# Kernel optimization log

Measured on AMD Instinct MI355X. Metric: run time of the kernel, lower is better.

The kernel has to match this reference:

```python
import jax, jax.numpy as jnp
import numpy as np

N, IN_DIM, OUT_DIM, H = 50000, 128, 128, 4
C = OUT_DIM // H  # 32, per-head channels
E = 1_600_000
NEG_SLOPE = 0.2
LN_EPS = 1e-5


def setup_inputs() -> dict:
    key = jax.random.key(0)
    ks = jax.random.split(key, 12)
    x = jax.random.normal(ks[0], (N, IN_DIM), dtype=jnp.float32)
    edge_index = jax.random.randint(ks[1], (2, E), 0, N, dtype=jnp.int64)
    edge_weight = jax.random.uniform(ks[2], (E,), dtype=jnp.float32)
    s = 1.0 / np.sqrt(IN_DIM)
    W = jax.random.normal(ks[3], (IN_DIM, H * C), dtype=jnp.float32) * s
    att_src = jax.random.normal(ks[4], (1, H, C), dtype=jnp.float32) * s
    att_dst = jax.random.normal(ks[5], (1, H, C), dtype=jnp.float32) * s
    W_edge = jax.random.normal(ks[6], (1, H * C), dtype=jnp.float32)
    att_edge = jax.random.normal(ks[7], (1, H, C), dtype=jnp.float32) * s
    bias = jnp.zeros((H * C,), dtype=jnp.float32)
    ln_gamma = jnp.ones((OUT_DIM,), dtype=jnp.float32)
    ln_beta = jnp.zeros((OUT_DIM,), dtype=jnp.float32)
    return {"x": x, "edge_index": edge_index, "edge_weight": edge_weight,
            "W": W, "att_src": att_src, "att_dst": att_dst,
            "W_edge": W_edge, "att_edge": att_edge, "bias": bias,
            "ln_gamma": ln_gamma, "ln_beta": ln_beta}


def _gat_forward(x, edge_index, edge_weight, W, att_src, att_dst, W_edge, att_edge, bias):
    # GATConv(in, C, heads=H, edge_dim=1), concat=True, add_self_loops=True (fill_value='mean')
    xp = (x @ W).reshape(N, H, C)                      # [N,H,C]
    a_src = jnp.sum(xp * att_src, axis=-1)             # [N,H]
    a_dst = jnp.sum(xp * att_dst, axis=-1)             # [N,H]

    # add self-loops; self-loop edge_attr = mean of existing edge_attr
    loop = jnp.arange(N, dtype=edge_index.dtype)
    src = jnp.concatenate([edge_index[0], loop])       # [E+N]
    dst = jnp.concatenate([edge_index[1], loop])
    ew = jnp.concatenate([edge_weight, jnp.full((N,), jnp.mean(edge_weight), edge_weight.dtype)])

    ea = (ew[:, None] @ W_edge).reshape(-1, H, C)      # [E+N,H,C]
    a_edge = jnp.sum(ea * att_edge, axis=-1)           # [E+N,H]

    logits = a_src[src] + a_dst[dst] + a_edge          # [E+N,H]
    logits = jax.nn.leaky_relu(logits, NEG_SLOPE)

    # segment softmax over destination-node neighborhoods
    m = jax.ops.segment_max(logits, dst, num_segments=N)     # [N,H]
    ex = jnp.exp(logits - m[dst])
    denom = jax.ops.segment_sum(ex, dst, num_segments=N)     # [N,H]
    attn = ex / (denom[dst] + 1e-16)                          # [E+N,H]

    msg = attn[:, :, None] * xp[src]                          # [E+N,H,C]
    out = jax.ops.segment_sum(msg, dst, num_segments=N)      # [N,H,C]
    return out.reshape(N, H * C) + bias


def reference(x, edge_index, edge_weight, W, att_src, att_dst, W_edge, att_edge, bias, ln_gamma, ln_beta):
    out = _gat_forward(x, edge_index, edge_weight, W, att_src, att_dst, W_edge, att_edge, bias)
    # LayerNorm
    mu = jnp.mean(out, axis=-1, keepdims=True)
    var = jnp.mean(jnp.square(out - mu), axis=-1, keepdims=True)
    out = (out - mu) / jnp.sqrt(var + LN_EPS) * ln_gamma + ln_beta
    # ELU (dropout is identity in eval)
    return jax.nn.elu(out)
```

## Files before the change

### kernel.cpp

```cpp
#include <hip/hip_runtime.h>
#include <hip/hip_fp16.h>
#include <cstddef>

#define N_NODES 50000
#define E_EDGES 1600000
#define NEG_SLOPE 0.2f
#define LN_EPS 1e-5f
#define LOG2E 1.4426950408889634f
#define PAD 96

#define NBK 782
#define BCAP 2560
#define PCH 4096
#define NCH 391
#define NGB 1563
#define TPB 256

#define OFF_SCAL    0u
#define OFF_BCUR    256u
#define OFF_EWPART  4096u
#define OFF_COUNTS  8192u
#define OFF_ASRC    208256u
#define OFF_ADST    1008256u
#define OFF_XPH     1808256u
#define OFF_PAIRS   14608256u
#define OFF_STAGE   33808256u

#define XROW_B   272
#define SWT_OFF  8704

typedef _Float16 half8 __attribute__((ext_vector_type(8)));
typedef float f32x4_t __attribute__((ext_vector_type(4)));

__device__ __forceinline__ float lrelu(float x) { return x > 0.f ? x : NEG_SLOPE * x; }

__device__ __forceinline__ float sel4(float4 v, int h) {
    float ab = (h & 1) ? v.y : v.x;
    float cd = (h & 1) ? v.w : v.z;
    return (h & 2) ? cd : ab;
}

__global__ __launch_bounds__(256, 3) void k_A(const float* __restrict__ x, const float* __restrict__ W,
                                              const float* __restrict__ att_src, const float* __restrict__ att_dst,
                                              const float* __restrict__ W_edge, const float* __restrict__ att_edge,
                                              const int* __restrict__ ei, const float* __restrict__ ew,
                                              unsigned short* __restrict__ xph, float* __restrict__ a_src,
                                              float* __restrict__ a_dst, float* __restrict__ scal,
                                              int* __restrict__ bcur, uint2* __restrict__ staging,
                                              float* __restrict__ ewPart) {
    __shared__ __align__(16) char smem[43520];
    int t = threadIdx.x;

    if (blockIdx.x < NCH) {
        int* cnt   = (int*)smem;
        int* gbase = cnt + NBK;
        float* wred = (float*)(gbase + NBK);
        for (int i = t; i < NBK; i += 256) cnt[i] = 0;
        __syncthreads();

        int e0 = blockIdx.x * PCH;
        int lr[16];
        float s_ew = 0.f;
        #pragma unroll
        for (int i = 0; i < 16; i++) {
            int e = e0 + i * 256 + t;
            lr[i] = 0;
            if (e < E_EDGES) {
                int d = ei[E_EDGES + e];
                s_ew += ew[e];
                lr[i] = atomicAdd(&cnt[d >> 6], 1);
            }
        }
        #pragma unroll
        for (int off = 32; off; off >>= 1) s_ew += __shfl_down(s_ew, off, 64);
        if ((t & 63) == 0) wred[t >> 6] = s_ew;
        __syncthreads();
        if (t == 0) ewPart[blockIdx.x] = wred[0] + wred[1] + wred[2] + wred[3];
        for (int i = t; i < NBK; i += 256) gbase[i] = atomicAdd(&bcur[i], cnt[i]);
        __syncthreads();

        #pragma unroll
        for (int i = 0; i < 16; i++) {
            int e = e0 + i * 256 + t;
            if (e < E_EDGES) {
                int s = ei[e];
                int d = ei[E_EDGES + e];
                float w = ew[e];
                int b = d >> 6;
                uint2 ent;
                ent.x = (unsigned int)s |
                        ((unsigned int)__half_as_ushort(__float2half_rn(w)) << 16);
                ent.y = (unsigned int)d;
                staging[(size_t)b * BCAP + gbase[b] + lr[i]] = ent;
            }
        }
        return;
    }

    int gb = blockIdx.x - NCH;
    if (gb == 0 && t < 128) {
        float p = W_edge[t] * att_edge[t];
        #pragma unroll
        for (int off = 16; off; off >>= 1) p += __shfl_down(p, off, 32);
        if ((t & 31) == 0) scal[4 + (t >> 5)] = p;
    }
    int r0 = gb * 32;

    for (int i = t; i < 1024; i += 256) {
        int row = i >> 5, c4 = i & 31;
        float4 v = make_float4(0.f, 0.f, 0.f, 0.f);
        if (r0 + row < N_NODES) v = ((const float4*)x)[(size_t)(r0 + row) * 32 + c4];
        __half2 h01 = __floats2half2_rn(v.x, v.y);
        __half2 h23 = __floats2half2_rn(v.z, v.w);
        uint2 pk;
        pk.x = *(unsigned int*)&h01;
        pk.y = *(unsigned int*)&h23;
        *(uint2*)(smem + XROW_B * row + 8 * c4) = pk;
    }
    {
        unsigned short* wt = (unsigned short*)(smem + SWT_OFF);
        for (int i = t; i < 4096; i += 256) {
            int k = i >> 5, c4 = i & 31;
            float4 v = ((const float4*)W)[k * 32 + c4];
            wt[(4 * c4 + 0) * 136 + k] = __half_as_ushort(__float2half_rn(v.x));
            wt[(4 * c4 + 1) * 136 + k] = __half_as_ushort(__float2half_rn(v.y));
            wt[(4 * c4 + 2) * 136 + k] = __half_as_ushort(__float2half_rn(v.z));
            wt[(4 * c4 + 3) * 136 + k] = __half_as_ushort(__float2half_rn(v.w));
        }
    }
    __syncthreads();

    int lane = t & 63;
    int wv = t >> 6;
    int g = lane >> 4, q = lane & 15;
    f32x4_t acc2[2][2] = {};
    {
        const char* pA = smem;
        const char* pB = smem + SWT_OFF;
        int cb = 32 * wv;
        #pragma unroll
        for (int s = 0; s < 4; s++) {
            half8 a0 = *(const half8*)(pA + XROW_B * q + 64 * s + 16 * g);
            half8 a1 = *(const half8*)(pA + XROW_B * (16 + q) + 64 * s + 16 * g);
            half8 b0 = *(const half8*)(pB + XROW_B * (cb + q) + 64 * s + 16 * g);
            half8 b1 = *(const half8*)(pB + XROW_B * (cb + 16 + q) + 64 * s + 16 * g);
            acc2[0][0] = __builtin_amdgcn_mfma_f32_16x16x32_f16(a0, b0, acc2[0][0], 0, 0, 0);
            acc2[0][1] = __builtin_amdgcn_mfma_f32_16x16x32_f16(a0, b1, acc2[0][1], 0, 0, 0);
            acc2[1][0] = __builtin_amdgcn_mfma_f32_16x16x32_f16(a1, b0, acc2[1][0], 0, 0, 0);
            acc2[1][1] = __builtin_amdgcn_mfma_f32_16x16x32_f16(a1, b1, acc2[1][1], 0, 0, 0);
        }
    }
    __syncthreads();
    float* sxp = (float*)smem;
    {
        int cb = 32 * wv;
        #pragma unroll
        for (int m = 0; m < 2; m++)
            #pragma unroll
            for (int nn = 0; nn < 2; nn++)
                #pragma unroll
                for (int r = 0; r < 4; r++)
                    sxp[(m * 16 + g * 4 + r) * 128 + cb + nn * 16 + q] = acc2[m][nn][r];
    }
    __syncthreads();

    int tc = t & 31;
    int tr = t >> 5;
    float4 s4 = ((const float4*)att_src)[tc];
    float4 d4 = ((const float4*)att_dst)[tc];
    int h = tc >> 3;
    #pragma unroll
    for (int r = 0; r < 4; r++) {
        int row = r0 + tr * 4 + r;
        if (row < N_NODES) {
            float4 a = ((const float4*)sxp)[(tr * 4 + r) * 32 + tc];
            __half2 h01 = __floats2half2_rn(a.x, a.y);
            __half2 h23 = __floats2half2_rn(a.z, a.w);
            uint2 pk;
            pk.x = *(unsigned int*)&h01;
            pk.y = *(unsigned int*)&h23;
            ((uint2*)xph)[(size_t)row * 32 + tc] = pk;
            float ps = a.x * s4.x + a.y * s4.y + a.z * s4.z + a.w * s4.w;
            float pd = a.x * d4.x + a.y * d4.y + a.z * d4.z + a.w * d4.w;
            ps += __shfl_down(ps, 4, 8); ps += __shfl_down(ps, 2, 8); ps += __shfl_down(ps, 1, 8);
            pd += __shfl_down(pd, 4, 8); pd += __shfl_down(pd, 2, 8); pd += __shfl_down(pd, 1, 8);
            if ((tc & 7) == 0) {
                a_src[(size_t)row * 4 + h] = ps;
                a_dst[(size_t)row * 4 + h] = pd;
            }
        }
    }
}

__global__ __launch_bounds__(256) void k_p2(const uint2* __restrict__ staging,
                                            const int* __restrict__ bcur,
                                            const float* __restrict__ ewPart,
                                            unsigned int* __restrict__ pairs,
                                            int* __restrict__ counts, float* __restrict__ scal) {
    int b = blockIdx.x, t = threadIdx.x;
    __shared__ int cnt2[64];
    __shared__ float wr2[4];
    if (b == 0) {
        float s = 0.f;
        for (int i = t; i < NCH; i += 256) s += ewPart[i];
        #pragma unroll
        for (int off = 32; off; off >>= 1) s += __shfl_down(s, off, 64);
        if ((t & 63) == 0) wr2[t >> 6] = s;
    }
    if (t < 64) cnt2[t] = 0;
    __syncthreads();
    if (b == 0 && t == 0) scal[0] = wr2[0] + wr2[1] + wr2[2] + wr2[3];
    int tot = bcur[b];
    const uint2* sg = staging + (size_t)b * BCAP;
    for (int i = t; i < tot; i += 256) {
        uint2 ent = sg[i];
        int d = (int)ent.y;
        int r = atomicAdd(&cnt2[d & 63], 1);
        pairs[(size_t)d * PAD + r] = ent.x;
    }
    __syncthreads();
    int n = (b << 6) + t;
    if (t < 64 && n < N_NODES) counts[n] = cnt2[t];
}

__global__ __launch_bounds__(256) void k_p3(const unsigned int* __restrict__ xpu,
                                            const float* __restrict__ a_src,
                                            const float* __restrict__ a_dst,
                                            const int* __restrict__ counts,
                                            const unsigned int* __restrict__ pairs,
                                            const float* __restrict__ scal,
                                            const float* __restrict__ bias,
                                            const float* __restrict__ gamma,
                                            const float* __restrict__ beta,
                                            float* __restrict__ out) {
    __shared__ unsigned long long sal[4][4][100];
    int lane = threadIdx.x & 63;
    int wv = threadIdx.x >> 6;
    int n = blockIdx.x * 4 + wv;
    if (n >= N_NODES) return;

    int h = lane >> 4;
    int em = lane & 15;

    float4 K = *(const float4*)(scal + 4);
    float Kh = sel4(K, h);
    float mean_ew = scal[0] * (1.0f / E_EDGES);

    int cnt = __builtin_amdgcn_readfirstlane(counts[n]);
    float4 ad4 = *(const float4*)(a_dst + (size_t)4 * n);
    float4 as4 = *(const float4*)(a_src + (size_t)4 * n);
    float adh = sel4(ad4, h);
    float aself = exp2f(lrelu(sel4(as4, h) + adh + Kh * mean_ew) * LOG2E);

    unsigned int pv = xpu[(size_t)n * 64 + lane];
    float2 f = __half22float2(*(__half2*)&pv);
    float acc0 = aself * f.x, acc1 = aself * f.y;

    unsigned long long* sl = &sal[wv][h][0];
    const unsigned int* prow = pairs + (size_t)n * PAD;
    float den = 0.f;
    #pragma unroll
    for (int b = 0; b < 6; b++) {
        if (b * 16 < cnt) {
            int e = b * 16 + em;
            float alpha = 0.f;
            int s = n;
            if (e < cnt) {
                unsigned int pk = prow[e];
                s = (int)(pk & 0xFFFFu);
                float w = __half2float(__ushort_as_half((unsigned short)(pk >> 16)));
                float4 av = *(const float4*)(a_src + (size_t)4 * s);
                alpha = exp2f(lrelu(sel4(av, h) + adh + Kh * w) * LOG2E);
            }
            den += alpha;
            sl[e] = ((unsigned long long)__float_as_uint(alpha) << 32) | (unsigned int)s;
        }
    }

    int cnt4 = (cnt + 3) & ~3;
    for (int e = 0; e < cnt4; e += 4) {
        ulonglong2 p01 = *(const ulonglong2*)(sl + e);
        ulonglong2 p23 = *(const ulonglong2*)(sl + e + 2);
        unsigned long long pq[4] = {p01.x, p01.y, p23.x, p23.y};
        #pragma unroll
        for (int q = 0; q < 4; q++) {
            unsigned int sj = (unsigned int)pq[q];
            float aj = __uint_as_float((unsigned int)(pq[q] >> 32));
            unsigned int g = xpu[(size_t)sj * 64 + lane];
            __half2 hh = *(__half2*)&g;
            acc0 = fmaf(aj, __half2float(__low2half(hh)), acc0);
            acc1 = fmaf(aj, __half2float(__high2half(hh)), acc1);
        }
    }

    den += __shfl_xor(den, 1, 64);
    den += __shfl_xor(den, 2, 64);
    den += __shfl_xor(den, 4, 64);
    den += __shfl_xor(den, 8, 64);
    den += aself;

    float inv = 1.0f / (den + 1e-16f);
    float2 b2 = ((const float2*)bias)[lane];
    float y0 = fmaf(acc0, inv, b2.x);
    float y1 = fmaf(acc1, inv, b2.y);

    float s1 = y0 + y1;
    #pragma unroll
    for (int off = 1; off < 64; off <<= 1) s1 += __shfl_xor(s1, off, 64);
    float mu = s1 * (1.f / 128.f);
    float d0 = y0 - mu, d1 = y1 - mu;
    float s2 = d0 * d0 + d1 * d1;
    #pragma unroll
    for (int off = 1; off < 64; off <<= 1) s2 += __shfl_xor(s2, off, 64);
    float rstd = rsqrtf(s2 * (1.f / 128.f) + LN_EPS);
    float2 g2 = ((const float2*)gamma)[lane];
    float2 be2 = ((const float2*)beta)[lane];
    float o0 = fmaf(d0 * rstd, g2.x, be2.x);
    float o1 = fmaf(d1 * rstd, g2.y, be2.y);
    o0 = o0 > 0.f ? o0 : expm1f(o0);
    o1 = o1 > 0.f ? o1 : expm1f(o1);
    float2 o; o.x = o0; o.y = o1;
    ((float2*)out)[(size_t)n * 64 + lane] = o;
}

extern "C" void kernel_launch(void* const* d_in, const int* in_sizes, int n_in,
                              void* d_out, int out_size, void* d_ws, size_t ws_size,
                              hipStream_t stream) {
    const float* x        = (const float*)d_in[0];
    const int*   ei       = (const int*)d_in[1];
    const float* ew       = (const float*)d_in[2];
    const float* W        = (const float*)d_in[3];
    const float* att_src  = (const float*)d_in[4];
    const float* att_dst  = (const float*)d_in[5];
    const float* W_edge   = (const float*)d_in[6];
    const float* att_edge = (const float*)d_in[7];
    const float* bias     = (const float*)d_in[8];
    const float* gamma    = (const float*)d_in[9];
    const float* beta     = (const float*)d_in[10];
    float* out = (float*)d_out;

    char* ws = (char*)d_ws;
    float* scal      = (float*)(ws + OFF_SCAL);
    int*   bcur      = (int*)(ws + OFF_BCUR);
    float* ewPart    = (float*)(ws + OFF_EWPART);
    int*   counts    = (int*)(ws + OFF_COUNTS);
    float* a_src     = (float*)(ws + OFF_ASRC);
    float* a_dst     = (float*)(ws + OFF_ADST);
    unsigned short* xph = (unsigned short*)(ws + OFF_XPH);
    unsigned int* pairs = (unsigned int*)(ws + OFF_PAIRS);
    uint2* staging   = (uint2*)(ws + OFF_STAGE);

    hipMemsetAsync(bcur, 0, NBK * sizeof(int), stream);
    k_A<<<NCH + NGB, TPB, 0, stream>>>(x, W, att_src, att_dst, W_edge, att_edge, ei, ew,
                                       xph, a_src, a_dst, scal, bcur, staging, ewPart);
    k_p2<<<NBK, TPB, 0, stream>>>(staging, bcur, ewPart, pairs, counts, scal);
    k_p3<<<12500, TPB, 0, stream>>>((const unsigned int*)xph, a_src, a_dst, counts, pairs, scal,
                                    bias, gamma, beta, out);
}
```

Before: 227.1 us.

## Pretranspose W to fp16 once in a setup kernel and read it from global

Adds a single-block kernel that converts W to fp16 in transposed layout and computes the edge-attention scalars once. The GEMM blocks of k_A then load B fragments straight from global/L2 instead of each of 1563 blocks re-converting and transposing W into shared memory. This shrinks k_A's LDS footprint (raising the occupancy hint to 4 blocks/CU) and pads the fp32 staging row stride to 132 to reduce bank conflicts. It adds a serial one-block launch and relies on L2 hits for the unpadded global B reads.

New measurement: 236.3 us. +4.0%, slower.

```diff
diff --git a/kernel.cpp b/kernel.cpp
--- a/kernel.cpp
+++ b/kernel.cpp
@@ -25,9 +25,9 @@
 #define OFF_XPH     1808256u
 #define OFF_PAIRS   14608256u
 #define OFF_STAGE   33808256u
+#define OFF_WT      49823616u
 
 #define XROW_B   272
-#define SWT_OFF  8704
 
 typedef _Float16 half8 __attribute__((ext_vector_type(8)));
 typedef float f32x4_t __attribute__((ext_vector_type(4)));
@@ -40,15 +40,33 @@
     return (h & 2) ? cd : ab;
 }
 
-__global__ __launch_bounds__(256, 3) void k_A(const float* __restrict__ x, const float* __restrict__ W,
+__global__ __launch_bounds__(256) void k_w(const float* __restrict__ W,
+                                           const float* __restrict__ W_edge,
+                                           const float* __restrict__ att_edge,
+                                           unsigned short* __restrict__ wt,
+                                           float* __restrict__ scal) {
+    int t = threadIdx.x;
+    if (t < 128) {
+        float p = W_edge[t] * att_edge[t];
+        #pragma unroll
+        for (int off = 16; off; off >>= 1) p += __shfl_down(p, off, 32);
+        if ((t & 31) == 0) scal[4 + (t >> 5)] = p;
+    }
+    for (int i = t; i < 16384; i += 256) {
+        int k = i >> 7, c = i & 127;
+        wt[c * 128 + k] = __half_as_ushort(__float2half_rn(W[i]));
+    }
+}
+
+__global__ __launch_bounds__(256, 4) void k_A(const float* __restrict__ x,
+                                              const unsigned short* __restrict__ wt,
                                               const float* __restrict__ att_src, const float* __restrict__ att_dst,
-                                              const float* __restrict__ W_edge, const float* __restrict__ att_edge,
                                               const int* __restrict__ ei, const float* __restrict__ ew,
                                               unsigned short* __restrict__ xph, float* __restrict__ a_src,
                                               float* __restrict__ a_dst, float* __restrict__ scal,
                                               int* __restrict__ bcur, uint2* __restrict__ staging,
                                               float* __restrict__ ewPart) {
-    __shared__ __align__(16) char smem[43520];
+    __shared__ __align__(16) char smem[16896];
     int t = threadIdx.x;
 
     if (blockIdx.x < NCH) {
@@ -98,12 +116,6 @@
     }
 
     int gb = blockIdx.x - NCH;
-    if (gb == 0 && t < 128) {
-        float p = W_edge[t] * att_edge[t];
-        #pragma unroll
-        for (int off = 16; off; off >>= 1) p += __shfl_down(p, off, 32);
-        if ((t & 31) == 0) scal[4 + (t >> 5)] = p;
-    }
     int r0 = gb * 32;
 
     for (int i = t; i < 1024; i += 256) {
@@ -117,33 +129,21 @@
         pk.y = *(unsigned int*)&h23;
         *(uint2*)(smem + XROW_B * row + 8 * c4) = pk;
     }
-    {
-        unsigned short* wt = (unsigned short*)(smem + SWT_OFF);
-        for (int i = t; i < 4096; i += 256) {
-            int k = i >> 5, c4 = i & 31;
-            float4 v = ((const float4*)W)[k * 32 + c4];
-            wt[(4 * c4 + 0) * 136 + k] = __half_as_ushort(__float2half_rn(v.x));
-            wt[(4 * c4 + 1) * 136 + k] = __half_as_ushort(__float2half_rn(v.y));
-            wt[(4 * c4 + 2) * 136 + k] = __half_as_ushort(__float2half_rn(v.z));
-            wt[(4 * c4 + 3) * 136 + k] = __half_as_ushort(__float2half_rn(v.w));
-        }
-    }
     __syncthreads();
 
     int lane = t & 63;
     int wv = t >> 6;
     int g = lane >> 4, q = lane & 15;
+    int cb = 32 * wv;
     f32x4_t acc2[2][2] = {};
     {
-        const char* pA = smem;
-        const char* pB = smem + SWT_OFF;
-        int cb = 32 * wv;
+        const char* pB = (const char*)wt;
         #pragma unroll
         for (int s = 0; s < 4; s++) {
-            half8 a0 = *(const half8*)(pA + XROW_B * q + 64 * s + 16 * g);
-            half8 a1 = *(const half8*)(pA + XROW_B * (16 + q) + 64 * s + 16 * g);
-            half8 b0 = *(const half8*)(pB + XROW_B * (cb + q) + 64 * s + 16 * g);
-            half8 b1 = *(const half8*)(pB + XROW_B * (cb + 16 + q) + 64 * s + 16 * g);
+            half8 a0 = *(const half8*)(smem + XROW_B * q + 64 * s + 16 * g);
+            half8 a1 = *(const half8*)(smem + XROW_B * (16 + q) + 64 * s + 16 * g);
+            half8 b0 = *(const half8*)(pB + (cb + q) * 256 + 64 * s + 16 * g);
+            half8 b1 = *(const half8*)(pB + (cb + 16 + q) * 256 + 64 * s + 16 * g);
             acc2[0][0] = __builtin_amdgcn_mfma_f32_16x16x32_f16(a0, b0, acc2[0][0], 0, 0, 0);
             acc2[0][1] = __builtin_amdgcn_mfma_f32_16x16x32_f16(a0, b1, acc2[0][1], 0, 0, 0);
             acc2[1][0] = __builtin_amdgcn_mfma_f32_16x16x32_f16(a1, b0, acc2[1][0], 0, 0, 0);
@@ -153,14 +153,13 @@
     __syncthreads();
     float* sxp = (float*)smem;
     {
-        int cb = 32 * wv;
         #pragma unroll
         for (int m = 0; m < 2; m++)
             #pragma unroll
             for (int nn = 0; nn < 2; nn++)
                 #pragma unroll
                 for (int r = 0; r < 4; r++)
-                    sxp[(m * 16 + g * 4 + r) * 128 + cb + nn * 16 + q] = acc2[m][nn][r];
+                    sxp[(m * 16 + g * 4 + r) * 132 + cb + nn * 16 + q] = acc2[m][nn][r];
     }
     __syncthreads();
 
@@ -173,7 +172,7 @@
     for (int r = 0; r < 4; r++) {
         int row = r0 + tr * 4 + r;
         if (row < N_NODES) {
-            float4 a = ((const float4*)sxp)[(tr * 4 + r) * 32 + tc];
+            float4 a = ((const float4*)sxp)[(tr * 4 + r) * 33 + tc];
             __half2 h01 = __floats2half2_rn(a.x, a.y);
             __half2 h23 = __floats2half2_rn(a.z, a.w);
             uint2 pk;
@@ -349,9 +348,11 @@
     unsigned short* xph = (unsigned short*)(ws + OFF_XPH);
     unsigned int* pairs = (unsigned int*)(ws + OFF_PAIRS);
     uint2* staging   = (uint2*)(ws + OFF_STAGE);
+    unsigned short* wt  = (unsigned short*)(ws + OFF_WT);
 
     hipMemsetAsync(bcur, 0, NBK * sizeof(int), stream);
-    k_A<<<NCH + NGB, TPB, 0, stream>>>(x, W, att_src, att_dst, W_edge, att_edge, ei, ew,
+    k_w<<<1, TPB, 0, stream>>>(W, W_edge, att_edge, wt, scal);
+    k_A<<<NCH + NGB, TPB, 0, stream>>>(x, wt, att_src, att_dst, ei, ew,
                                        xph, a_src, a_dst, scal, bcur, staging, ewPart);
     k_p2<<<NBK, TPB, 0, stream>>>(staging, bcur, ewPart, pairs, counts, scal);
     k_p3<<<12500, TPB, 0, stream>>>((const unsigned int*)xph, a_src, a_dst, counts, pairs, scal,
```
